# Kernel tuning notes

Hardware: AMD Instinct MI355X
Metric: run time of the kernel (lower is better)

Reference implementation:

```python
import jax, jax.numpy as jnp
import numpy as np
from functools import partial


def conv2d(x, w, b=None, stride=1):
    # torch Conv2d(k=3, padding=1, stride=stride), NCHW / OIHW
    y = jax.lax.conv_general_dilated(
        x, w, window_strides=(stride, stride), padding=((1, 1), (1, 1)),
        dimension_numbers=("NCHW", "OIHW", "NCHW"))
    if b is not None:
        y = y + b[None, :, None, None]
    return y


def conv_offset2d(x, ow):
    """ConvOffset2D: conv -> (B*C,H,W,2) offsets -> bilinear sample of x at grid+offset."""
    B, C, H, W = x.shape
    off = conv2d(x, ow)                      # (B, 2C, H, W), no bias
    off = off.reshape(B * C, H, W, 2)        # faithful raw reshape as in torch code
    xb = x.reshape(B * C, H, W)
    rr, cc = jnp.meshgrid(jnp.arange(H, dtype=x.dtype), jnp.arange(W, dtype=x.dtype), indexing="ij")
    r = jnp.clip(off[..., 0] + rr, 0.0, H - 1)   # row coords, clamped
    c = jnp.clip(off[..., 1] + cc, 0.0, W - 1)   # col coords, clamped
    r0 = jnp.floor(r); r1 = jnp.ceil(r)
    c0 = jnp.floor(c); c1 = jnp.ceil(c)
    bi = jnp.arange(B * C)[:, None, None]

    def gather(ri, ci):
        return xb[bi, ri.astype(jnp.int32), ci.astype(jnp.int32)]

    v_lt = gather(r0, c0)  # (floor r, floor c)
    v_rb = gather(r1, c1)  # (ceil r,  ceil c)
    v_lb = gather(r0, c1)  # (floor r, ceil c)
    v_rt = gather(r1, c0)  # (ceil r,  floor c)
    fr = r - r0
    fc = c - c0
    vt = v_lt + (v_rt - v_lt) * fr
    vb = v_lb + (v_rb - v_lb) * fr
    out = vt + (vb - vt) * fc
    return out.reshape(B, C, H, W)


def setup_inputs() -> dict:
    key = jax.random.key(0)
    ks = jax.random.split(key, 16)
    C = 32
    B, H, W = 16, 256, 256

    def conv_w(k, co, ci):
        return jax.random.normal(k, (co, ci, 3, 3), jnp.float32) * (1.0 / np.sqrt(ci * 9))

    inp = {
        "x": jax.random.normal(ks[0], (B, C, H, W), jnp.float32),
        "w1": conv_w(ks[1], C, C),       "b1": jnp.zeros((C,), jnp.float32),
        "ow1": jax.random.normal(ks[2], (2 * C, C, 3, 3), jnp.float32) * 0.01,
        "w2": conv_w(ks[3], 2 * C, C),   "b2": jnp.zeros((2 * C,), jnp.float32),
        "ow2": jax.random.normal(ks[4], (4 * C, 2 * C, 3, 3), jnp.float32) * 0.01,
        "w3": conv_w(ks[5], C, 2 * C),   "b3": jnp.zeros((C,), jnp.float32),
        "ow3": jax.random.normal(ks[6], (2 * C, C, 3, 3), jnp.float32) * 0.01,
        "w4": conv_w(ks[7], C, C),       "b4": jnp.zeros((C,), jnp.float32),
    }
    return inp


def reference(x, w1, b1, ow1, w2, b2, ow2, w3, b3, ow3, w4, b4):
    # Dropout layers are identity in eval mode.
    h = jax.nn.relu(conv2d(x, w1, b1))                 # (B, C, H, W)
    h = conv_offset2d(h, ow1)
    h = jax.nn.relu(conv2d(h, w2, b2, stride=2))       # (B, 2C, H/2, W/2)
    h = conv_offset2d(h, ow2)
    h = jax.nn.relu(conv2d(h, w3, b3, stride=2))       # (B, C, H/4, W/4)
    h = conv_offset2d(h, ow3)
    h = jax.nn.relu(conv2d(h, w4, b4, stride=2))       # (B, C, H/8, W/8)
    return jnp.mean(h, axis=(2, 3), keepdims=True)     # global avg pool -> (B, C, 1, 1)
```

## Files before the change

kernel.cpp:

```cpp
#include <hip/hip_runtime.h>

typedef short short8 __attribute__((ext_vector_type(8)));
typedef float f32x4 __attribute__((ext_vector_type(4)));

__device__ __forceinline__ unsigned short f2b(float f) {
    unsigned u = __float_as_uint(f);
    u += 0x7fffu + ((u >> 16) & 1u);
    return (unsigned short)(u >> 16);
}
__device__ __forceinline__ float b2f(unsigned short h) {
    return __uint_as_float(((unsigned)h) << 16);
}

template <int C_IN, int C_OUT, int NW, int DEFORM>
__global__ __launch_bounds__(NW * 64) void conv_s1_mfma(
    const unsigned short* __restrict__ in, const unsigned short* __restrict__ wT,
    const float* __restrict__ bias, unsigned short* __restrict__ out,
    int H, int W, int relu)
{
    constexpr int LDSTR  = C_IN + 8;
    constexpr int KSTEPS = C_IN / 32;
    constexpr int CH8    = C_IN / 8;
    constexpr int COPB   = 32 * (NW / 4);
    static_assert(!DEFORM || COPB == 64, "deform fusion expects 64 conv ch/block");
    constexpr int SSTR   = 40;
    constexpr int S_CONV = 18 * 18 * LDSTR;
    constexpr int S_SMP  = DEFORM ? 4 * 100 * SSTR : 0;
    constexpr int S_A    = (S_CONV > S_SMP) ? S_CONV : S_SMP;
    __shared__ __align__(16) unsigned short s_in[S_A];
    __shared__ __align__(16) unsigned short s_off[DEFORM ? 16 * 16 * 64 : 8];

    const int tid   = threadIdx.x;
    const int wave  = tid >> 6;
    const int wv    = wave & 3;
    const int csub  = wave >> 2;
    const int lane  = tid & 63;
    const int mlane = lane & 15;
    const int quad  = lane >> 4;

    const int nCo  = C_OUT / COPB;
    const int b    = blockIdx.z / nCo;
    const int coB  = (blockIdx.z - b * nCo) * COPB + csub * 32;
    const int row0 = blockIdx.y * 16;
    const int col0 = blockIdx.x * 16;

    for (int idx = tid; idx < 18 * 18 * CH8; idx += NW * 64) {
        int pixel = idx / CH8;
        int ch    = (idx - pixel * CH8) * 8;
        int pr    = pixel / 18;
        int pc    = pixel - pr * 18;
        int gr = row0 - 1 + pr, gc = col0 - 1 + pc;
        ulonglong2 v; v.x = 0; v.y = 0;
        if ((unsigned)gr < (unsigned)H && (unsigned)gc < (unsigned)W)
            v = *(const ulonglong2*)&in[((b * H + gr) * W + gc) * C_IN + ch];
        *(ulonglong2*)&s_in[pixel * LDSTR + ch] = v;
    }
    __syncthreads();

    f32x4 acc[2][4];
    #pragma unroll
    for (int mt = 0; mt < 2; ++mt)
        #pragma unroll
        for (int t = 0; t < 4; ++t) acc[mt][t] = (f32x4)(0.f);

    #pragma unroll 1
    for (int kk = 0; kk < KSTEPS; ++kk) {
        short8 A[2][9];
        #pragma unroll
        for (int mt = 0; mt < 2; ++mt)
            #pragma unroll
            for (int tap = 0; tap < 9; ++tap)
                A[mt][tap] = *(const short8*)&wT[(tap * C_OUT + coB + mt * 16 + mlane) * C_IN
                                                 + kk * 32 + quad * 8];

        const unsigned short* sb =
            &s_in[(wv * 4 * 18 + mlane) * LDSTR + kk * 32 + quad * 8];
        #pragma unroll
        for (int t = 0; t < 4; ++t) {
            #pragma unroll
            for (int tap = 0; tap < 9; ++tap) {
                const int dy = tap / 3, dx = tap % 3;
                short8 Bf = *(const short8*)&sb[((t + dy) * 18 + dx) * LDSTR];
                acc[0][t] = __builtin_amdgcn_mfma_f32_16x16x32_bf16(A[0][tap], Bf, acc[0][t], 0, 0, 0);
                acc[1][t] = __builtin_amdgcn_mfma_f32_16x16x32_bf16(A[1][tap], Bf, acc[1][t], 0, 0, 0);
            }
        }
    }

    if (!DEFORM) {
        #pragma unroll
        for (int mt = 0; mt < 2; ++mt) {
            const int cb = coB + mt * 16 + quad * 4;
            float4 bv;
            if (bias) bv = *(const float4*)&bias[cb]; else { bv.x = bv.y = bv.z = bv.w = 0.f; }
            #pragma unroll
            for (int t = 0; t < 4; ++t) {
                const int row = row0 + wv * 4 + t, col = col0 + mlane;
                float o0 = acc[mt][t][0] + bv.x, o1 = acc[mt][t][1] + bv.y;
                float o2 = acc[mt][t][2] + bv.z, o3 = acc[mt][t][3] + bv.w;
                if (relu) {
                    o0 = fmaxf(o0, 0.f); o1 = fmaxf(o1, 0.f);
                    o2 = fmaxf(o2, 0.f); o3 = fmaxf(o3, 0.f);
                }
                ushort4 pk; pk.x = f2b(o0); pk.y = f2b(o1); pk.z = f2b(o2); pk.w = f2b(o3);
                *(ushort4*)&out[((b * H + row) * W + col) * C_OUT + cb] = pk;
            }
        }
    } else {
        const int zb    = blockIdx.z - b * nCo;
        const int zbase = zb * 32;
        const int Hh = H >> 1, Wh = W >> 1;
        const int r8 = blockIdx.y * 8, c8 = blockIdx.x * 8;

        __syncthreads();

        #pragma unroll
        for (int mt = 0; mt < 2; ++mt) {
            const int cb  = csub * 32 + mt * 16 + quad * 4;
            const int swc = cb ^ ((mlane & 7) << 3);
            #pragma unroll
            for (int t = 0; t < 4; ++t) {
                ushort4 pk;
                pk.x = f2b(acc[mt][t][0]); pk.y = f2b(acc[mt][t][1]);
                pk.z = f2b(acc[mt][t][2]); pk.w = f2b(acc[mt][t][3]);
                *(ushort4*)&s_off[((wv * 4 + t) * 16 + mlane) * 64 + swc] = pk;
            }
        }

        for (int idx = tid; idx < 1600; idx += NW * 64) {
            const int pixel = idx >> 2;
            const int chq   = (idx & 3) * 8;
            const int reg   = pixel / 100;
            const int rem   = pixel - reg * 100;
            const int rr_   = rem / 10;
            const int cc_   = rem - rr_ * 10;
            int gr = r8 + (reg >> 1) * Hh - 1 + rr_;
            int gc = c8 + (reg & 1)  * Wh - 1 + cc_;
            gr = gr < 0 ? 0 : (gr > H - 1 ? H - 1 : gr);
            gc = gc < 0 ? 0 : (gc > W - 1 ? W - 1 : gc);
            *(ulonglong2*)&s_in[pixel * SSTR + chq] =
                *(const ulonglong2*)&in[((b * H + gr) * W + gc) * C_IN + zbase + chq];
        }
        __syncthreads();

        const int ci   = tid & 31;
        const int slot = tid >> 5;
        const unsigned short* xb = in  + (long)b * H * W * C_IN + zbase + ci;
        unsigned short*       ob = out + (long)b * H * W * C_IN + zbase + ci;
        const float Hm1 = (float)(H - 1), Wm1 = (float)(W - 1);

        #pragma unroll 4
        for (int s = 0; s < 8; ++s) {
            const int pos = slot + s * 16;
            const int rl  = pos >> 4;
            const int cl  = (pos >> 1) & 7;
            const int chf = pos & 1;
            const int lr  = rl * 2 + chf;
            const int lc  = cl * 2;
            const int bix = (lr * 16 + lc) * 64;
            const ushort2 roP = *(const ushort2*)&s_off[bix +      ((2 * ci) ^ ((lc & 7) << 3))];
            const ushort2 coP = *(const ushort2*)&s_off[bix + 64 + ((2 * ci) ^ (((lc + 1) & 7) << 3))];
            #pragma unroll
            for (int ih = 0; ih < 2; ++ih) {
                const int R0 = r8 + ih * Hh, C0 = c8 + chf * Wh;
                const int rowg = R0 + rl, cg = C0 + cl;
                const float rr = __builtin_amdgcn_fmed3f(
                    b2f(ih ? roP.y : roP.x) + (float)rowg, 0.f, Hm1);
                const float cc = __builtin_amdgcn_fmed3f(
                    b2f(ih ? coP.y : coP.x) + (float)cg, 0.f, Wm1);
                const int irf = (int)rr, icf = (int)cc;
                const float fr = rr - (float)irf;
                const float fc = cc - (float)icf;
                const int lr0 = irf - R0 + 1;
                const int lc0 = icf - C0 + 1;
                float v00, v01, v10, v11;
                if ((unsigned)lr0 <= 8u && (unsigned)lc0 <= 8u) {
                    const unsigned short* sp =
                        &s_in[((ih * 2 + chf) * 100 + lr0 * 10 + lc0) * SSTR + ci];
                    v00 = b2f(sp[0]);
                    v01 = b2f(sp[SSTR]);
                    v10 = b2f(sp[10 * SSTR]);
                    v11 = b2f(sp[11 * SSTR]);
                } else {
                    const int dr1 = (fr > 0.f) ? 1 : 0;
                    const int dc1 = (fc > 0.f) ? 1 : 0;
                    const int idx00 = (irf * W + icf) * C_IN;
                    const int dr = dr1 * W * C_IN, dc = dc1 * C_IN;
                    v00 = b2f(xb[idx00]);
                    v01 = b2f(xb[idx00 + dc]);
                    v10 = b2f(xb[idx00 + dr]);
                    v11 = b2f(xb[idx00 + dr + dc]);
                }
                const float vt = v00 + (v10 - v00) * fr;
                const float vb = v01 + (v11 - v01) * fr;
                const float rs = vt + (vb - vt) * fc;
                ob[(rowg * W + cg) * C_IN] = f2b(rs);
            }
        }
    }
}

template <int C_IN, int C_OUT, int NW>
__global__ __launch_bounds__(NW * 64) void conv_s2_mfma(
    const unsigned short* __restrict__ in, const unsigned short* __restrict__ wT,
    const float* __restrict__ bias, unsigned short* __restrict__ out,
    int H_in, int W_in, int relu)
{
    constexpr int LDSTR  = C_IN + 8;
    constexpr int KSTEPS = C_IN / 32;
    constexpr int CH8    = C_IN / 8;
    constexpr int COPB   = 32 * (NW / 4);
    __shared__ unsigned short s_in[17 * 17 * LDSTR];

    const int tid   = threadIdx.x;
    const int wave  = tid >> 6;
    const int wv    = wave & 3;
    const int csub  = wave >> 2;
    const int lane  = tid & 63;
    const int mlane = lane & 15;
    const int quad  = lane >> 4;

    const int H_out = H_in >> 1, W_out = W_in >> 1;
    const int nCo   = C_OUT / COPB;
    const int b     = blockIdx.z / nCo;
    const int coB   = (blockIdx.z - b * nCo) * COPB + csub * 32;
    const int orow0 = blockIdx.y * 8, ocol0 = blockIdx.x * 8;
    const int irow0 = orow0 * 2 - 1,  icol0 = ocol0 * 2 - 1;

    for (int idx = tid; idx < 17 * 17 * CH8; idx += NW * 64) {
        int pixel = idx / CH8;
        int ch    = (idx - pixel * CH8) * 8;
        int pr    = pixel / 17;
        int pc    = pixel - pr * 17;
        int gr = irow0 + pr, gc = icol0 + pc;
        ulonglong2 v; v.x = 0; v.y = 0;
        if ((unsigned)gr < (unsigned)H_in && (unsigned)gc < (unsigned)W_in)
            v = *(const ulonglong2*)&in[((b * H_in + gr) * W_in + gc) * C_IN + ch];
        *(ulonglong2*)&s_in[pixel * LDSTR + ch] = v;
    }
    __syncthreads();

    f32x4 acc[2];
    acc[0] = (f32x4)(0.f); acc[1] = (f32x4)(0.f);

    const int plr = wv * 2 + (mlane >> 3);
    const int plc = mlane & 7;

    #pragma unroll 1
    for (int kk = 0; kk < KSTEPS; ++kk) {
        short8 A[2][9];
        #pragma unroll
        for (int mt = 0; mt < 2; ++mt)
            #pragma unroll
            for (int tap = 0; tap < 9; ++tap)
                A[mt][tap] = *(const short8*)&wT[(tap * C_OUT + coB + mt * 16 + mlane) * C_IN
                                                 + kk * 32 + quad * 8];

        const unsigned short* sb0 =
            &s_in[(plr * 2 * 17 + plc * 2) * LDSTR + kk * 32 + quad * 8];
        #pragma unroll
        for (int tap = 0; tap < 9; ++tap) {
            const int dy = tap / 3, dx = tap % 3;
            short8 Bf = *(const short8*)&sb0[(dy * 17 + dx) * LDSTR];
            acc[0] = __builtin_amdgcn_mfma_f32_16x16x32_bf16(A[0][tap], Bf, acc[0], 0, 0, 0);
            acc[1] = __builtin_amdgcn_mfma_f32_16x16x32_bf16(A[1][tap], Bf, acc[1], 0, 0, 0);
        }
    }

    const int row = orow0 + plr, col = ocol0 + plc;
    #pragma unroll
    for (int mt = 0; mt < 2; ++mt) {
        const int cb = coB + mt * 16 + quad * 4;
        float4 bv;
        if (bias) bv = *(const float4*)&bias[cb]; else { bv.x = bv.y = bv.z = bv.w = 0.f; }
        float o0 = acc[mt][0] + bv.x, o1 = acc[mt][1] + bv.y;
        float o2 = acc[mt][2] + bv.z, o3 = acc[mt][3] + bv.w;
        if (relu) {
            o0 = fmaxf(o0, 0.f); o1 = fmaxf(o1, 0.f);
            o2 = fmaxf(o2, 0.f); o3 = fmaxf(o3, 0.f);
        }
        ushort4 pk; pk.x = f2b(o0); pk.y = f2b(o1); pk.z = f2b(o2); pk.w = f2b(o3);
        *(ushort4*)&out[((b * H_out + row) * W_out + col) * C_OUT + cb] = pk;
    }
}

__global__ __launch_bounds__(256) void nchw2nhwc(
    const float* __restrict__ x, unsigned short* __restrict__ out, int HW)
{
    __shared__ float s[32][65];
    const int b = blockIdx.y, p0 = blockIdx.x * 64;
    const int tid = threadIdx.x;
    #pragma unroll
    for (int k = 0; k < 8; ++k) {
        int e = tid + k * 256, ci = e >> 6, p = e & 63;
        s[ci][p] = x[(b * 32 + ci) * HW + p0 + p];
    }
    __syncthreads();
    #pragma unroll
    for (int k = 0; k < 8; ++k) {
        int e = tid + k * 256, p = e >> 5, ci = e & 31;
        out[(b * HW + p0 + p) * 32 + ci] = f2b(s[ci][p]);
    }
}

struct WTArgs {
    const float* src[7];
    unsigned short* dst[7];
    int co[7], ci[7], n[7];
};
__global__ __launch_bounds__(256) void wtrans_all(WTArgs a)
{
    const int i = blockIdx.x * 256 + threadIdx.x;
    #pragma unroll
    for (int s = 0; s < 7; ++s) {
        if (i < a.n[s]) {
            const int ci  = i % a.ci[s];
            const int rr  = i / a.ci[s];
            const int co  = rr % a.co[s];
            const int tap = rr / a.co[s];
            a.dst[s][i] = f2b(a.src[s][(co * a.ci[s] + ci) * 9 + tap]);
        }
    }
}

__global__ __launch_bounds__(256) void avgpool_nhwc(
    const unsigned short* __restrict__ in, float* __restrict__ out)
{
    const int b = blockIdx.x, tid = threadIdx.x;
    const int ci = tid & 31, pg = tid >> 5;
    float s = 0.f;
    for (int k = 0; k < 128; ++k) {
        int p = pg * 128 + k;
        s += b2f(in[(b * 1024 + p) * 32 + ci]);
    }
    __shared__ float red[8][32];
    red[pg][ci] = s;
    __syncthreads();
    if (tid < 32) {
        float t = 0.f;
        #pragma unroll
        for (int j = 0; j < 8; ++j) t += red[j][tid];
        out[b * 32 + tid] = t * (1.f / 1024.f);
    }
}

__global__ __launch_bounds__(256) void sentinel(float* out, int n, float v)
{
    int i = blockIdx.x * 256 + threadIdx.x;
    if (i < n) out[i] = v;
}

extern "C" void kernel_launch(void* const* d_in, const int* in_sizes, int n_in,
                              void* d_out, int out_size, void* d_ws, size_t ws_size,
                              hipStream_t stream) {
    (void)in_sizes; (void)n_in; (void)out_size;
    const float* x   = (const float*)d_in[0];
    const float* w1  = (const float*)d_in[1];
    const float* b1  = (const float*)d_in[2];
    const float* ow1 = (const float*)d_in[3];
    const float* w2  = (const float*)d_in[4];
    const float* b2  = (const float*)d_in[5];
    const float* ow2 = (const float*)d_in[6];
    const float* w3  = (const float*)d_in[7];
    const float* b3  = (const float*)d_in[8];
    const float* ow3 = (const float*)d_in[9];
    const float* w4  = (const float*)d_in[10];
    const float* b4  = (const float*)d_in[11];
    float* out = (float*)d_out;
    unsigned short* wsu = (unsigned short*)d_ws;

    const size_t XB = 0;
    const size_t HA = 33554432;
    const size_t DC = 134217728;
    const size_t WB = 167772160;
    const size_t total_us = WB + 165888;
    if (ws_size < total_us * 2) {
        sentinel<<<2, 256, 0, stream>>>(out, 512, 12345.0f);
        return;
    }
    unsigned short* xb = wsu + XB;
    unsigned short* hA = wsu + HA;
    unsigned short* dC = wsu + DC;
    unsigned short* wt1  = wsu + WB;
    unsigned short* owt1 = wt1 + 9216;
    unsigned short* wt2  = owt1 + 18432;
    unsigned short* owt2 = wt2 + 18432;
    unsigned short* wt3  = owt2 + 73728;
    unsigned short* owt3 = wt3 + 18432;
    unsigned short* wt4  = owt3 + 18432;

    WTArgs wa;
    wa.src[0] = w1;  wa.dst[0] = wt1;  wa.co[0] = 32;  wa.ci[0] = 32; wa.n[0] = 9216;
    wa.src[1] = ow1; wa.dst[1] = owt1; wa.co[1] = 64;  wa.ci[1] = 32; wa.n[1] = 18432;
    wa.src[2] = w2;  wa.dst[2] = wt2;  wa.co[2] = 64;  wa.ci[2] = 32; wa.n[2] = 18432;
    wa.src[3] = ow2; wa.dst[3] = owt2; wa.co[3] = 128; wa.ci[3] = 64; wa.n[3] = 73728;
    wa.src[4] = w3;  wa.dst[4] = wt3;  wa.co[4] = 32;  wa.ci[4] = 64; wa.n[4] = 18432;
    wa.src[5] = ow3; wa.dst[5] = owt3; wa.co[5] = 64;  wa.ci[5] = 32; wa.n[5] = 18432;
    wa.src[6] = w4;  wa.dst[6] = wt4;  wa.co[6] = 32;  wa.ci[6] = 32; wa.n[6] = 9216;
    wtrans_all<<<288, 256, 0, stream>>>(wa);

    nchw2nhwc<<<dim3(1024, 16), 256, 0, stream>>>(x, xb, 65536);

    conv_s1_mfma<32, 32, 4, 0><<<dim3(16, 16, 16), 256, 0, stream>>>(xb, wt1, b1, hA, 256, 256, 1);
    conv_s1_mfma<32, 64, 8, 1><<<dim3(16, 16, 16), 512, 0, stream>>>(hA, owt1, nullptr, dC, 256, 256, 0);

    conv_s2_mfma<32, 64, 8><<<dim3(16, 16, 16), 512, 0, stream>>>(dC, wt2, b2, hA, 256, 256, 1);
    conv_s1_mfma<64, 128, 8, 1><<<dim3(8, 8, 32), 512, 0, stream>>>(hA, owt2, nullptr, dC, 128, 128, 0);

    conv_s2_mfma<64, 32, 4><<<dim3(8, 8, 16), 256, 0, stream>>>(dC, wt3, b3, hA, 128, 128, 1);
    conv_s1_mfma<32, 64, 8, 1><<<dim3(4, 4, 16), 512, 0, stream>>>(hA, owt3, nullptr, dC, 64, 64, 0);

    conv_s2_mfma<32, 32, 4><<<dim3(4, 4, 16), 256, 0, stream>>>(dC, wt4, b4, hA, 64, 64, 1);
    avgpool_nhwc<<<16, 256, 0, stream>>>(hA, out);
}
```

Measured before the change: 550.0 us.

## Prefetch deform sample tile into registers early and retile weights for coalesced loads

In the fused deformable conv kernel, the global loads for the sampling tile are issued into registers before the MFMA loop and written to LDS afterward, so their latency overlaps the convolution compute. Separately, the transposed weight layout is rearranged into 16-output by 8-input chunks so that each wave's A-fragment loads read contiguous memory. The prefetch costs up to four extra 128-bit registers per thread, which may reduce occupancy.

```diff
diff --git a/kernel.cpp b/kernel.cpp
--- a/kernel.cpp
+++ b/kernel.cpp
@@ -11,6 +11,7 @@
 __device__ __forceinline__ float b2f(unsigned short h) {
     return __uint_as_float(((unsigned)h) << 16);
 }
+
 
 template <int C_IN, int C_OUT, int NW, int DEFORM>
 __global__ __launch_bounds__(NW * 64) void conv_s1_mfma(
@@ -55,6 +56,30 @@
             v = *(const ulonglong2*)&in[((b * H + gr) * W + gc) * C_IN + ch];
         *(ulonglong2*)&s_in[pixel * LDSTR + ch] = v;
     }
+
+    ulonglong2 sv[4];
+    if (DEFORM) {
+        const int zbase = (blockIdx.z - b * nCo) * 32;
+        const int Hh = H >> 1, Wh = W >> 1;
+        const int r8 = blockIdx.y * 8, c8 = blockIdx.x * 8;
+        #pragma unroll
+        for (int j = 0; j < 4; ++j) {
+            const int idx = tid + j * (NW * 64);
+            if (idx < 1600) {
+                const int pixel = idx >> 2;
+                const int chq   = (idx & 3) * 8;
+                const int reg   = pixel / 100;
+                const int rem   = pixel - reg * 100;
+                const int rr_   = rem / 10;
+                const int cc_   = rem - rr_ * 10;
+                int gr = r8 + (reg >> 1) * Hh - 1 + rr_;
+                int gc = c8 + (reg & 1)  * Wh - 1 + cc_;
+                gr = gr < 0 ? 0 : (gr > H - 1 ? H - 1 : gr);
+                gc = gc < 0 ? 0 : (gc > W - 1 ? W - 1 : gc);
+                sv[j] = *(const ulonglong2*)&in[((b * H + gr) * W + gc) * C_IN + zbase + chq];
+            }
+        }
+    }
     __syncthreads();
 
     f32x4 acc[2][4];
@@ -70,8 +95,9 @@
         for (int mt = 0; mt < 2; ++mt)
             #pragma unroll
             for (int tap = 0; tap < 9; ++tap)
-                A[mt][tap] = *(const short8*)&wT[(tap * C_OUT + coB + mt * 16 + mlane) * C_IN
-                                                 + kk * 32 + quad * 8];
+                A[mt][tap] = *(const short8*)&wT[
+                    ((((tap * (C_OUT / 16) + (coB >> 4) + mt) * (C_IN / 8))
+                      + kk * 4 + quad) * 16 + mlane) * 8];
 
         const unsigned short* sb =
             &s_in[(wv * 4 * 18 + mlane) * LDSTR + kk * 32 + quad * 8];
@@ -126,20 +152,14 @@
                 *(ushort4*)&s_off[((wv * 4 + t) * 16 + mlane) * 64 + swc] = pk;
             }
         }
-
-        for (int idx = tid; idx < 1600; idx += NW * 64) {
-            const int pixel = idx >> 2;
-            const int chq   = (idx & 3) * 8;
-            const int reg   = pixel / 100;
-            const int rem   = pixel - reg * 100;
-            const int rr_   = rem / 10;
-            const int cc_   = rem - rr_ * 10;
-            int gr = r8 + (reg >> 1) * Hh - 1 + rr_;
-            int gc = c8 + (reg & 1)  * Wh - 1 + cc_;
-            gr = gr < 0 ? 0 : (gr > H - 1 ? H - 1 : gr);
-            gc = gc < 0 ? 0 : (gc > W - 1 ? W - 1 : gc);
-            *(ulonglong2*)&s_in[pixel * SSTR + chq] =
-                *(const ulonglong2*)&in[((b * H + gr) * W + gc) * C_IN + zbase + chq];
+        #pragma unroll
+        for (int j = 0; j < 4; ++j) {
+            const int idx = tid + j * (NW * 64);
+            if (idx < 1600) {
+                const int pixel = idx >> 2;
+                const int chq   = (idx & 3) * 8;
+                *(ulonglong2*)&s_in[pixel * SSTR + chq] = sv[j];
+            }
         }
         __syncthreads();
 
@@ -253,8 +273,9 @@
         for (int mt = 0; mt < 2; ++mt)
             #pragma unroll
             for (int tap = 0; tap < 9; ++tap)
-                A[mt][tap] = *(const short8*)&wT[(tap * C_OUT + coB + mt * 16 + mlane) * C_IN
-                                                 + kk * 32 + quad * 8];
+                A[mt][tap] = *(const short8*)&wT[
+                    ((((tap * (C_OUT / 16) + (coB >> 4) + mt) * (C_IN / 8))
+                      + kk * 4 + quad) * 16 + mlane) * 8];
 
         const unsigned short* sb0 =
             &s_in[(plr * 2 * 17 + plc * 2) * LDSTR + kk * 32 + quad * 8];
@@ -314,10 +335,18 @@
     #pragma unroll
     for (int s = 0; s < 7; ++s) {
         if (i < a.n[s]) {
-            const int ci  = i % a.ci[s];
-            const int rr  = i / a.ci[s];
-            const int co  = rr % a.co[s];
-            const int tap = rr / a.co[s];
+            const int nci8  = a.ci[s] >> 3;
+            const int nco16 = a.co[s] >> 4;
+            const int ci_in  = i & 7;
+            const int t1     = i >> 3;
+            const int co_in  = t1 & 15;
+            const int t2     = t1 >> 4;
+            const int ci_grp = t2 % nci8;
+            const int t3     = t2 / nci8;
+            const int co_blk = t3 % nco16;
+            const int tap    = t3 / nco16;
+            const int co = co_blk * 16 + co_in;
+            const int ci = ci_grp * 8 + ci_in;
             a.dst[s][i] = f2b(a.src[s][(co * a.ci[s] + ci) * 9 + tap]);
         }
     }
```

Measured after the change: 504.0 us, median of 2. 8.4% less time.
